# Kernel tuning notes

Hardware: AMD Instinct MI355X
Metric: run time of the kernel (lower is better)

## Reference

```python
import jax, jax.numpy as jnp
import numpy as np

EMBED_DIM = 512
HEAD_NUM = 8
HEAD_DIM = EMBED_DIM // HEAD_NUM


def setup_inputs() -> dict:
    key = jax.random.key(0)
    ks = jax.random.split(key, 13)
    B, S, E = 4, 2048, EMBED_DIM
    inp = {
        "key": jax.random.normal(ks[0], (B, S, E), dtype=jnp.float32),
        "value": jax.random.normal(ks[1], (B, S, E), dtype=jnp.float32),
        "query": jax.random.normal(ks[2], (B, S, E), dtype=jnp.float32),
        "mask": jax.random.randint(ks[3], (B, 1, S, S), 0, 2, dtype=jnp.int32),
    }
    # Linear params (torch nn.Linear: y = x @ W.T + b); init with small scale
    def lin(kw, kb):
        W = jax.random.normal(kw, (E, E), dtype=jnp.float32) * (1.0 / np.sqrt(E))
        b = jax.random.normal(kb, (E,), dtype=jnp.float32) * 0.01
        return W, b
    inp["Wq"], inp["bq"] = lin(ks[4], ks[5])
    inp["Wk"], inp["bk"] = lin(ks[6], ks[7])
    inp["Wv"], inp["bv"] = lin(ks[8], ks[9])
    inp["Wo"], inp["bo"] = lin(ks[10], ks[11])
    return inp


def reference(key, value, query, mask, Wq, bq, Wk, bk, Wv, bv, Wo, bo):
    B, Q, E = query.shape
    K = key.shape[1]
    H, D = HEAD_NUM, HEAD_DIM
    # projections (torch Linear: x @ W.T + b)
    q = (query @ Wq.T + bq).reshape(B, Q, H, D)
    k = (key @ Wk.T + bk).reshape(B, K, H, D)
    v = (value @ Wv.T + bv).reshape(B, K, H, D)
    # scores [B,H,Q,K]
    scores = jnp.einsum("bqhd,bkhd->bhqk", q, k)
    # mask BEFORE scaling, exactly as the torch module does
    scores = jnp.where(mask == 0, jnp.float32(-1e20), scores)
    # NOTE: scales by sqrt(embed_dim), not sqrt(head_dim) -- faithful to source
    attn = jax.nn.softmax(scores / jnp.sqrt(jnp.float32(E)), axis=3)
    out = jnp.einsum("bhqk,bkhd->bqhd", attn, v).reshape(B, Q, E)
    return out @ Wo.T + bo
```

## Files before the change

kernel.cpp:

```cpp
#include <hip/hip_runtime.h>
#include <hip/hip_fp16.h>
#include <stdint.h>

#define EMBED 512
#define HEADS 8
#define HDIM 64
#define BATCH 4
#define SEQ 2048
#define MTOT (BATCH*SEQ)

typedef _Float16 half8_t __attribute__((ext_vector_type(8)));
typedef _Float16 half4_t __attribute__((ext_vector_type(4)));
typedef __fp16 fp16x2_t __attribute__((ext_vector_type(2)));
typedef float floatx4 __attribute__((ext_vector_type(4)));

typedef const __attribute__((address_space(1))) void* gp1_t;
typedef __attribute__((address_space(3))) void* sp3_t;

__device__ __forceinline__ void gload_lds16(const void* g, void* s) {
  __builtin_amdgcn_global_load_lds((gp1_t)g, (sp3_t)s, 16, 0, 0);
}

__global__ __launch_bounds__(256) void prep_kernel(
    const float* __restrict__ wq, const float* __restrict__ wk,
    const float* __restrict__ wv, const float* __restrict__ wo,
    const int* __restrict__ mask,
    _Float16* hwq, _Float16* hwk, _Float16* hwv, _Float16* hwo,
    unsigned long long* __restrict__ bits) {
  int z = blockIdx.y;
  if (z == 4) {
    int lane = threadIdx.x & 63;
    int wid = (blockIdx.x * 256 + threadIdx.x) >> 6;
    int nw = (gridDim.x * 256) >> 6;
    int ngroups = BATCH * SEQ * SEQ / 64 / 4;
    for (int g = wid; g < ngroups; g += nw) {
      const int* base = mask + (size_t)g * 256;
      int v0 = base[lane];
      int v1 = base[64 + lane];
      int v2 = base[128 + lane];
      int v3 = base[192 + lane];
      unsigned long long b0 = __ballot(v0 != 0);
      unsigned long long b1 = __ballot(v1 != 0);
      unsigned long long b2 = __ballot(v2 != 0);
      unsigned long long b3 = __ballot(v3 != 0);
      if (lane == 0) {
        ulonglong4 w4 = { b0, b1, b2, b3 };
        *(ulonglong4*)&bits[(size_t)g * 4] = w4;
      }
    }
    return;
  }
  const float* src = (z == 0) ? wq : (z == 1) ? wk : (z == 2) ? wv : wo;
  _Float16* dst = (z == 0) ? hwq : (z == 1) ? hwk : (z == 2) ? hwv : hwo;
  int n4 = EMBED * EMBED / 4;
  int stride = gridDim.x * blockDim.x;
  for (int i = blockIdx.x * blockDim.x + threadIdx.x; i < n4; i += stride) {
    float4 f = ((const float4*)src)[i];
    half4_t h = { (_Float16)f.x, (_Float16)f.y, (_Float16)f.z, (_Float16)f.w };
    ((half4_t*)dst)[i] = h;
  }
}

struct GemmParams {
  const void* A[4];
  const void* W[4];
  int a32[4], w32[4];
  const float* bias[4];
  _Float16* outH[3];
  float* outF;
  float oscale[4];
  int mode_base;
};

__global__ __launch_bounds__(256) void proj_gemm(GemmParams p) {
  int mode = p.mode_base + blockIdx.z;
  const void* __restrict__ A = p.A[mode];
  const void* __restrict__ W = p.W[mode];
  const bool a32 = p.a32[mode] != 0, w32 = p.w32[mode] != 0;
  const float* __restrict__ bias = p.bias[mode];
  float oscale = p.oscale[mode];
  int m0, n0;
  if (mode == 2) { m0 = blockIdx.y * 128; n0 = blockIdx.x * 128; }
  else           { m0 = blockIdx.x * 128; n0 = blockIdx.y * 128; }

  __shared__ __align__(16) _Float16 As[128 * 64];
  __shared__ __align__(16) _Float16 Bs[128 * 64];

  int t = threadIdx.x;
  int lane = t & 63;
  int wv = t >> 6;
  int wr = wv >> 1, wc = wv & 1;
  int l15 = lane & 15, l4 = lane >> 4;

  floatx4 acc[4][4] = {};

  for (int kt = 0; kt < EMBED; kt += 64) {
    if (!a32) {
#pragma unroll
      for (int i = 0; i < 4; i++) {
        int c = i * 256 + t;
        int row = c >> 3, col8 = (c & 7) * 8;
        gload_lds16((const _Float16*)A + (size_t)(m0 + row) * EMBED + kt + col8,
                    (void*)&As[c * 8]);
      }
    } else {
#pragma unroll
      for (int i = 0; i < 4; i++) {
        int c = i * 256 + t;
        int row = c >> 3, col8 = (c & 7) * 8;
        const float* s = (const float*)A + (size_t)(m0 + row) * EMBED + kt + col8;
        float4 f0 = *(const float4*)s;
        float4 f1 = *(const float4*)(s + 4);
        half8_t hh = { (_Float16)f0.x, (_Float16)f0.y, (_Float16)f0.z, (_Float16)f0.w,
                       (_Float16)f1.x, (_Float16)f1.y, (_Float16)f1.z, (_Float16)f1.w };
        *(half8_t*)&As[c * 8] = hh;
      }
    }
    if (!w32) {
#pragma unroll
      for (int i = 0; i < 4; i++) {
        int c = i * 256 + t;
        int row = c >> 3, col8 = (c & 7) * 8;
        gload_lds16((const _Float16*)W + (size_t)(n0 + row) * EMBED + kt + col8,
                    (void*)&Bs[c * 8]);
      }
    } else {
#pragma unroll
      for (int i = 0; i < 4; i++) {
        int c = i * 256 + t;
        int row = c >> 3, col8 = (c & 7) * 8;
        const float* s = (const float*)W + (size_t)(n0 + row) * EMBED + kt + col8;
        float4 f0 = *(const float4*)s;
        float4 f1 = *(const float4*)(s + 4);
        half8_t hh = { (_Float16)f0.x, (_Float16)f0.y, (_Float16)f0.z, (_Float16)f0.w,
                       (_Float16)f1.x, (_Float16)f1.y, (_Float16)f1.z, (_Float16)f1.w };
        *(half8_t*)&Bs[c * 8] = hh;
      }
    }
    __syncthreads();

    half8_t af[4][2], bf[4][2];
#pragma unroll
    for (int i = 0; i < 4; i++)
#pragma unroll
      for (int kc = 0; kc < 2; kc++) {
        af[i][kc] = *(const half8_t*)&As[(wr * 64 + i * 16 + l15) * 64 + kc * 32 + l4 * 8];
        bf[i][kc] = *(const half8_t*)&Bs[(wc * 64 + i * 16 + l15) * 64 + kc * 32 + l4 * 8];
      }
    __builtin_amdgcn_s_setprio(1);
#pragma unroll
    for (int i = 0; i < 4; i++)
#pragma unroll
      for (int j = 0; j < 4; j++)
#pragma unroll
        for (int kc = 0; kc < 2; kc++)
          acc[i][j] = __builtin_amdgcn_mfma_f32_16x16x32_f16(af[i][kc], bf[j][kc], acc[i][j], 0, 0, 0);
    __builtin_amdgcn_s_setprio(0);
    __syncthreads();
  }

#pragma unroll
  for (int i = 0; i < 4; i++)
#pragma unroll
    for (int j = 0; j < 4; j++) {
      int n = n0 + wc * 64 + j * 16 + l15;
#pragma unroll
      for (int r = 0; r < 4; r++) {
        int m = m0 + wr * 64 + i * 16 + l4 * 4 + r;
        if (mode == 2) {
          float val = acc[i][j][r] + bias[m];
          int hh = m >> 6, dd = m & 63;
          int bb = n >> 11, ss = n & 2047;
          p.outH[2][((size_t)(bb * 8 + hh) * 64 + dd) * SEQ + ss] = (_Float16)val;
        } else {
          float val = (acc[i][j][r] + bias[n]) * oscale;
          if (mode < 2) {
            int b = m >> 11, s = m & 2047, h = n >> 6, d = n & 63;
            p.outH[mode][(((size_t)(b * 8 + h)) * SEQ + s) * HDIM + d] = (_Float16)val;
          } else {
            p.outF[(size_t)m * EMBED + n] = val;
          }
        }
      }
    }
}

__global__ __launch_bounds__(256) void flash_kernel(
    const _Float16* __restrict__ qh, const _Float16* __restrict__ kh,
    const _Float16* __restrict__ vt, const unsigned long long* __restrict__ mbits,
    _Float16* __restrict__ attn_h) {
  int qt = blockIdx.x;
  int bh = blockIdx.y;
  int b = bh >> 3, h = bh & 7;
  int t = threadIdx.x, lane = t & 63, w = t >> 6;
  int l15 = lane & 15, l4 = lane >> 4;

  __shared__ __align__(16) _Float16 Klds[2][64 * 64];
  __shared__ __align__(16) _Float16 Vlds[2][64 * 64];
  __shared__ __align__(16) _Float16 Plds[64 * 64];

  const size_t headoff = ((size_t)(b * 8 + h)) * SEQ * HDIM;
  const _Float16* Kg = kh + headoff;
  const _Float16* Vg = vt + headoff;
  int q0 = qt * 64 + w * 16;

  half8_t qf[2];
#pragma unroll
  for (int kc = 0; kc < 2; kc++)
    qf[kc] = *(const half8_t*)&qh[headoff + (size_t)(q0 + l15) * HDIM + kc * 32 + l4 * 8];

  floatx4 acc[4] = {};
  float lst = 0.f;
  const unsigned long long* mrow = mbits + ((size_t)(b * SEQ) + q0 + l15) * (SEQ / 64);

  auto stage = [&](int buf, int kt) {
#pragma unroll
    for (int i = 0; i < 2; i++) {
      int c = i * 256 + t;
      int row = c >> 3;
      int col16 = (c & 7) ^ (row & 7);
      gload_lds16((const char*)(Kg + (size_t)(kt * 64 + row) * HDIM) + col16 * 16,
                  (char*)&Klds[buf][0] + c * 16);
    }
#pragma unroll
    for (int i = 0; i < 2; i++) {
      int c = i * 256 + t;
      int row = c >> 3;
      int col16 = (c & 7) ^ (row & 7);
      gload_lds16((const char*)(Vg + (size_t)row * SEQ + kt * 64) + col16 * 16,
                  (char*)&Vlds[buf][0] + c * 16);
    }
  };

  stage(0, 0);
  unsigned long long rb = mrow[0];
  int cur = 0;
  for (int kt = 0; kt < SEQ / 64; kt++) {
    __syncthreads();
    if (kt + 1 < SEQ / 64) stage(cur ^ 1, kt + 1);
    unsigned long long rb_next = (kt + 1 < SEQ / 64) ? mrow[kt + 1] : 0ull;

    const char* Kb = (const char*)&Klds[cur][0];
    const char* Vb = (const char*)&Vlds[cur][0];

    floatx4 s[4] = {};
    __builtin_amdgcn_s_setprio(1);
#pragma unroll
    for (int nt = 0; nt < 4; nt++)
#pragma unroll
      for (int kc = 0; kc < 2; kc++) {
        int krow = nt * 16 + l15;
        half8_t kf = *(const half8_t*)(Kb + krow * 128 + (((kc * 4 + l4) ^ (krow & 7)) * 16));
        s[nt] = __builtin_amdgcn_mfma_f32_16x16x32_f16(kf, qf[kc], s[nt], 0, 0, 0);
      }
    __builtin_amdgcn_s_setprio(0);

    float e[4][4];
    float rsn[4];
#pragma unroll
    for (int nt = 0; nt < 4; nt++) {
      unsigned nib = (unsigned)(rb >> (nt * 16 + l4 * 4)) & 0xFu;
      float e0 = __expf(s[nt][0]); e0 = (nib & 1u) ? e0 : 0.f;
      float e1 = __expf(s[nt][1]); e1 = (nib & 2u) ? e1 : 0.f;
      float e2 = __expf(s[nt][2]); e2 = (nib & 4u) ? e2 : 0.f;
      float e3 = __expf(s[nt][3]); e3 = (nib & 8u) ? e3 : 0.f;
      e[nt][0] = e0; e[nt][1] = e1; e[nt][2] = e2; e[nt][3] = e3;
      rsn[nt] = (e0 + e1) + (e2 + e3);
    }
    float rs = (rsn[0] + rsn[1]) + (rsn[2] + rsn[3]);
    rs += __shfl_xor(rs, 16);
    rs += __shfl_xor(rs, 32);
    lst += rs;
    rb = rb_next;

    int prow = w * 16 + l15;
#pragma unroll
    for (int nt = 0; nt < 4; nt++) {
      fp16x2_t h01 = __builtin_amdgcn_cvt_pkrtz(e[nt][0], e[nt][1]);
      fp16x2_t h23 = __builtin_amdgcn_cvt_pkrtz(e[nt][2], e[nt][3]);
      uint2 pk = { __builtin_bit_cast(unsigned, h01), __builtin_bit_cast(unsigned, h23) };
      int colb = (nt * 32 + l4 * 8) ^ ((l15 & 7) << 4);
      *(uint2*)((char*)Plds + prow * 128 + colb) = pk;
    }

    __builtin_amdgcn_s_setprio(1);
#pragma unroll
    for (int kc = 0; kc < 2; kc++) {
      half8_t pa = *(const half8_t*)((char*)Plds + prow * 128 + (((kc * 4 + l4) ^ (l15 & 7)) * 16));
#pragma unroll
      for (int dt = 0; dt < 4; dt++) {
        int vrow = dt * 16 + l15;
        half8_t vb = *(const half8_t*)(Vb + vrow * 128 + (((kc * 4 + l4) ^ (vrow & 7)) * 16));
        acc[dt] = __builtin_amdgcn_mfma_f32_16x16x32_f16(pa, vb, acc[dt], 0, 0, 0);
      }
    }
    __builtin_amdgcn_s_setprio(0);
    cur ^= 1;
  }

  float li[4];
#pragma unroll
  for (int r = 0; r < 4; r++) li[r] = __shfl(lst, l4 * 4 + r);
#pragma unroll
  for (int dt = 0; dt < 4; dt++)
#pragma unroll
    for (int r = 0; r < 4; r++) {
      int q = q0 + l4 * 4 + r;
      float o = acc[dt][r] / li[r];
      attn_h[((size_t)(b * SEQ + q)) * EMBED + h * HDIM + dt * 16 + l15] = (_Float16)o;
    }
}

extern "C" void kernel_launch(void* const* d_in, const int* in_sizes, int n_in,
                              void* d_out, int out_size, void* d_ws, size_t ws_size,
                              hipStream_t stream) {
  const float* key   = (const float*)d_in[0];
  const float* value = (const float*)d_in[1];
  const float* query = (const float*)d_in[2];
  const int*   mask  = (const int*)d_in[3];
  const float* Wq = (const float*)d_in[4];  const float* bq = (const float*)d_in[5];
  const float* Wk = (const float*)d_in[6];  const float* bk = (const float*)d_in[7];
  const float* Wv = (const float*)d_in[8];  const float* bv = (const float*)d_in[9];
  const float* Wo = (const float*)d_in[10]; const float* bo = (const float*)d_in[11];

  char* ws = (char*)d_ws;
  _Float16* hwq = (_Float16*)(ws + 0);
  _Float16* hwk = (_Float16*)(ws + 524288);
  _Float16* hwv = (_Float16*)(ws + 1048576);
  _Float16* hwo = (_Float16*)(ws + 1572864);
  _Float16* qh  = (_Float16*)(ws + 2097152);
  _Float16* kh  = (_Float16*)(ws + 10485760);
  _Float16* vt  = (_Float16*)(ws + 18874368);
  _Float16* ah  = (_Float16*)(ws + 27262976);
  unsigned long long* mb = (unsigned long long*)(ws + 35651584);

  prep_kernel<<<dim3(512, 5), 256, 0, stream>>>(Wq, Wk, Wv, Wo, mask,
                                                hwq, hwk, hwv, hwo, mb);

  GemmParams gp;
  gp.A[0] = query; gp.a32[0] = 1; gp.W[0] = hwq;   gp.w32[0] = 0;
  gp.A[1] = key;   gp.a32[1] = 1; gp.W[1] = hwk;   gp.w32[1] = 0;
  gp.A[2] = hwv;   gp.a32[2] = 0; gp.W[2] = value; gp.w32[2] = 1;
  gp.A[3] = ah;    gp.a32[3] = 0; gp.W[3] = hwo;   gp.w32[3] = 0;
  gp.bias[0] = bq; gp.bias[1] = bk; gp.bias[2] = bv; gp.bias[3] = bo;
  gp.outH[0] = qh; gp.outH[1] = kh; gp.outH[2] = vt;
  gp.outF = (float*)d_out;
  gp.oscale[0] = 0.04419417382415922f;
  gp.oscale[1] = 1.f; gp.oscale[2] = 1.f; gp.oscale[3] = 1.f;
  gp.mode_base = 0;
  proj_gemm<<<dim3(64, 4, 3), 256, 0, stream>>>(gp);

  flash_kernel<<<dim3(32, 32), 256, 0, stream>>>(qh, kh, vt, mb, ah);

  gp.mode_base = 3;
  proj_gemm<<<dim3(64, 4, 1), 256, 0, stream>>>(gp);
}
```

Before: 304.8 us.

## Shrink projection GEMM tiles, double-buffer swizzled LDS, use exp2 softmax

The projection GEMM now uses 64x64 tiles with a 1D grid of 1024 blocks, double-buffered XOR-swizzled LDS and a single barrier per k-step. This is meant to fill more CUs and overlap loads with MFMA while reducing bank conflicts. The attention softmax switches to the hardware exp2 instruction, with log2(e) folded into the query scale. Smaller tiles lower data reuse per block and raise global traffic.

Result: no change. 303.0 us (-0.6%).

```diff
diff --git a/kernel.cpp b/kernel.cpp
--- a/kernel.cpp
+++ b/kernel.cpp
@@ -79,12 +79,13 @@
   const bool a32 = p.a32[mode] != 0, w32 = p.w32[mode] != 0;
   const float* __restrict__ bias = p.bias[mode];
   float oscale = p.oscale[mode];
+  int bx = blockIdx.x;
   int m0, n0;
-  if (mode == 2) { m0 = blockIdx.y * 128; n0 = blockIdx.x * 128; }
-  else           { m0 = blockIdx.x * 128; n0 = blockIdx.y * 128; }
-
-  __shared__ __align__(16) _Float16 As[128 * 64];
-  __shared__ __align__(16) _Float16 Bs[128 * 64];
+  if (mode == 2) { m0 = (bx & 7) * 64; n0 = (bx >> 3) * 64; }
+  else           { m0 = (bx >> 3) * 64; n0 = (bx & 7) * 64; }
+
+  __shared__ __align__(16) _Float16 As[2][64 * 64];
+  __shared__ __align__(16) _Float16 Bs[2][64 * 64];
 
   int t = threadIdx.x;
   int lane = t & 63;
@@ -92,81 +93,77 @@
   int wr = wv >> 1, wc = wv & 1;
   int l15 = lane & 15, l4 = lane >> 4;
 
-  floatx4 acc[4][4] = {};
-
-  for (int kt = 0; kt < EMBED; kt += 64) {
-    if (!a32) {
-#pragma unroll
-      for (int i = 0; i < 4; i++) {
-        int c = i * 256 + t;
-        int row = c >> 3, col8 = (c & 7) * 8;
-        gload_lds16((const _Float16*)A + (size_t)(m0 + row) * EMBED + kt + col8,
-                    (void*)&As[c * 8]);
-      }
-    } else {
-#pragma unroll
-      for (int i = 0; i < 4; i++) {
-        int c = i * 256 + t;
-        int row = c >> 3, col8 = (c & 7) * 8;
-        const float* s = (const float*)A + (size_t)(m0 + row) * EMBED + kt + col8;
+  floatx4 acc[2][2] = {};
+
+  auto stage = [&](int buf, int kt) {
+#pragma unroll
+    for (int i = 0; i < 2; i++) {
+      int c = i * 256 + t;
+      int row = c >> 3;
+      int cs = (c & 7) ^ (row & 7);
+      if (!a32) {
+        gload_lds16((const _Float16*)A + (size_t)(m0 + row) * EMBED + kt + cs * 8,
+                    (void*)&As[buf][c * 8]);
+      } else {
+        const float* s = (const float*)A + (size_t)(m0 + row) * EMBED + kt + cs * 8;
         float4 f0 = *(const float4*)s;
         float4 f1 = *(const float4*)(s + 4);
         half8_t hh = { (_Float16)f0.x, (_Float16)f0.y, (_Float16)f0.z, (_Float16)f0.w,
                        (_Float16)f1.x, (_Float16)f1.y, (_Float16)f1.z, (_Float16)f1.w };
-        *(half8_t*)&As[c * 8] = hh;
-      }
-    }
-    if (!w32) {
-#pragma unroll
-      for (int i = 0; i < 4; i++) {
-        int c = i * 256 + t;
-        int row = c >> 3, col8 = (c & 7) * 8;
-        gload_lds16((const _Float16*)W + (size_t)(n0 + row) * EMBED + kt + col8,
-                    (void*)&Bs[c * 8]);
-      }
-    } else {
-#pragma unroll
-      for (int i = 0; i < 4; i++) {
-        int c = i * 256 + t;
-        int row = c >> 3, col8 = (c & 7) * 8;
-        const float* s = (const float*)W + (size_t)(n0 + row) * EMBED + kt + col8;
+        *(half8_t*)&As[buf][c * 8] = hh;
+      }
+      if (!w32) {
+        gload_lds16((const _Float16*)W + (size_t)(n0 + row) * EMBED + kt + cs * 8,
+                    (void*)&Bs[buf][c * 8]);
+      } else {
+        const float* s = (const float*)W + (size_t)(n0 + row) * EMBED + kt + cs * 8;
         float4 f0 = *(const float4*)s;
         float4 f1 = *(const float4*)(s + 4);
         half8_t hh = { (_Float16)f0.x, (_Float16)f0.y, (_Float16)f0.z, (_Float16)f0.w,
                        (_Float16)f1.x, (_Float16)f1.y, (_Float16)f1.z, (_Float16)f1.w };
-        *(half8_t*)&Bs[c * 8] = hh;
-      }
-    }
+        *(half8_t*)&Bs[buf][c * 8] = hh;
+      }
+    }
+  };
+
+  stage(0, 0);
+  int cur = 0;
+  for (int kt = 0; kt < EMBED; kt += 64) {
     __syncthreads();
-
-    half8_t af[4][2], bf[4][2];
-#pragma unroll
-    for (int i = 0; i < 4; i++)
+    if (kt + 64 < EMBED) stage(cur ^ 1, kt + 64);
+
+    const char* Ab = (const char*)&As[cur][0];
+    const char* Bb = (const char*)&Bs[cur][0];
+    half8_t af[2][2], bf[2][2];
+#pragma unroll
+    for (int i = 0; i < 2; i++)
 #pragma unroll
       for (int kc = 0; kc < 2; kc++) {
-        af[i][kc] = *(const half8_t*)&As[(wr * 64 + i * 16 + l15) * 64 + kc * 32 + l4 * 8];
-        bf[i][kc] = *(const half8_t*)&Bs[(wc * 64 + i * 16 + l15) * 64 + kc * 32 + l4 * 8];
+        int arow = wr * 32 + i * 16 + l15;
+        int brow = wc * 32 + i * 16 + l15;
+        af[i][kc] = *(const half8_t*)(Ab + arow * 128 + (((kc * 4 + l4) ^ (arow & 7)) * 16));
+        bf[i][kc] = *(const half8_t*)(Bb + brow * 128 + (((kc * 4 + l4) ^ (brow & 7)) * 16));
       }
     __builtin_amdgcn_s_setprio(1);
 #pragma unroll
-    for (int i = 0; i < 4; i++)
-#pragma unroll
-      for (int j = 0; j < 4; j++)
+    for (int i = 0; i < 2; i++)
+#pragma unroll
+      for (int j = 0; j < 2; j++)
 #pragma unroll
         for (int kc = 0; kc < 2; kc++)
           acc[i][j] = __builtin_amdgcn_mfma_f32_16x16x32_f16(af[i][kc], bf[j][kc], acc[i][j], 0, 0, 0);
     __builtin_amdgcn_s_setprio(0);
-    __syncthreads();
+    cur ^= 1;
   }
 
 #pragma unroll
-  for (int i = 0; i < 4; i++)
-#pragma unroll
-    for (int j = 0; j < 4; j++) {
-      int n = n0 + wc * 64 + j * 16 + l15;
+  for (int i = 0; i < 2; i++)
+#pragma unroll
+    for (int j = 0; j < 2; j++) {
+      int n = n0 + wc * 32 + j * 16 + l15;
 #pragma unroll
       for (int r = 0; r < 4; r++) {
-        int m = m0 + wr * 64 + i * 16 + l4 * 4 + r;
+        int m = m0 + wr * 32 + i * 16 + l4 * 4 + r;
         if (mode == 2) {
           float val = acc[i][j][r] + bias[m];
           int hh = m >> 6, dd = m & 63;
@@ -260,10 +257,10 @@
 #pragma unroll
     for (int nt = 0; nt < 4; nt++) {
       unsigned nib = (unsigned)(rb >> (nt * 16 + l4 * 4)) & 0xFu;
-      float e0 = __expf(s[nt][0]); e0 = (nib & 1u) ? e0 : 0.f;
-      float e1 = __expf(s[nt][1]); e1 = (nib & 2u) ? e1 : 0.f;
-      float e2 = __expf(s[nt][2]); e2 = (nib & 4u) ? e2 : 0.f;
-      float e3 = __expf(s[nt][3]); e3 = (nib & 8u) ? e3 : 0.f;
+      float e0 = __builtin_amdgcn_exp2f(s[nt][0]); e0 = (nib & 1u) ? e0 : 0.f;
+      float e1 = __builtin_amdgcn_exp2f(s[nt][1]); e1 = (nib & 2u) ? e1 : 0.f;
+      float e2 = __builtin_amdgcn_exp2f(s[nt][2]); e2 = (nib & 4u) ? e2 : 0.f;
+      float e3 = __builtin_amdgcn_exp2f(s[nt][3]); e3 = (nib & 8u) ? e3 : 0.f;
       e[nt][0] = e0; e[nt][1] = e1; e[nt][2] = e2; e[nt][3] = e3;
       rsn[nt] = (e0 + e1) + (e2 + e3);
     }
@@ -345,13 +342,13 @@
   gp.bias[0] = bq; gp.bias[1] = bk; gp.bias[2] = bv; gp.bias[3] = bo;
   gp.outH[0] = qh; gp.outH[1] = kh; gp.outH[2] = vt;
   gp.outF = (float*)d_out;
-  gp.oscale[0] = 0.04419417382415922f;
+  gp.oscale[0] = 0.0637587160f;
   gp.oscale[1] = 1.f; gp.oscale[2] = 1.f; gp.oscale[3] = 1.f;
   gp.mode_base = 0;
-  proj_gemm<<<dim3(64, 4, 3), 256, 0, stream>>>(gp);
+  proj_gemm<<<dim3(1024, 1, 3), 256, 0, stream>>>(gp);
 
   flash_kernel<<<dim3(32, 32), 256, 0, stream>>>(qh, kh, vt, mb, ah);
 
   gp.mode_base = 3;
-  proj_gemm<<<dim3(64, 4, 1), 256, 0, stream>>>(gp);
-}
+  proj_gemm<<<dim3(1024, 1, 1), 256, 0, stream>>>(gp);
+}
```
